# Performance work log

Hardware: AMD Instinct MI355X
Metric: run time of the kernel (lower is better)

## Reference

```python
import jax, jax.numpy as jnp
import numpy as np

N = 100000      # nodes
E = 3200000     # edges (avg degree 32)
DU = 256        # unary_channels
DP = 256        # pairwise_channels (== out_channels, required by fusion cat)
H = 64          # hidden_channels = out_channels // 4
DO = 256        # out_channels
STEPS = 1
EPS = 1e-5      # BatchNorm eps (torch default)


def _bn(h, gamma, beta):
    # BatchNorm1d, training-mode batch stats (biased variance, as torch normalizes)
    mu = jnp.mean(h, axis=0)
    var = jnp.var(h, axis=0)
    return gamma * (h - mu) * jax.lax.rsqrt(var + EPS) + beta


def setup_inputs() -> dict:
    key = jax.random.key(0)
    ks = jax.random.split(key, 12)
    edge_index = jax.random.randint(ks[0], (2, E), 0, N, dtype=jnp.int64)
    return {
        "x": jax.random.normal(ks[1], (N, DU), dtype=jnp.float32),
        "y": jax.random.normal(ks[2], (N, DP), dtype=jnp.float32),
        "pos": jax.random.normal(ks[3], (N, 3), dtype=jnp.float32),
        "edge_index": edge_index,
        "Wu": jax.random.normal(ks[4], (DU, H), dtype=jnp.float32) / np.sqrt(DU),
        "gu": jnp.ones((H,), jnp.float32), "bu": jnp.zeros((H,), jnp.float32),
        "Wp": jax.random.normal(ks[5], (DP, H), dtype=jnp.float32) / np.sqrt(DP),
        "gp": jnp.ones((H,), jnp.float32), "bp": jnp.zeros((H,), jnp.float32),
        "c": jnp.eye(H, dtype=jnp.float32) + 0.1 * jax.random.normal(ks[6], (H, H), dtype=jnp.float32),
        "Wm": jax.random.normal(ks[7], (H, DO), dtype=jnp.float32) / np.sqrt(H),
        "gm": jnp.ones((DO,), jnp.float32), "bm": jnp.zeros((DO,), jnp.float32),
        "Wf": jax.random.normal(ks[8], (2 * DO, DO), dtype=jnp.float32) / np.sqrt(2 * DO),
        "gf": jnp.ones((DO,), jnp.float32), "bf": jnp.zeros((DO,), jnp.float32),
    }


def reference(x, y, pos, edge_index, Wu, gu, bu, Wp, gp, bp, c, Wm, gm, bm, Wf, gf, bf):
    i, j = edge_index[0], edge_index[1]
    # unary / pairwise embeddings (Linear no-bias + BN)
    xu = _bn(x @ Wu, gu, bu)                      # [N, H]
    su = _bn(y @ Wp, gp, bp)                      # [N, H]
    # edge logits: -||s_i - s_j||^2, softmax grouped by destination i
    d = su[i] - su[j]                             # [E, H]
    logit = -jnp.sum(d * d, axis=1, keepdims=True)  # [E, 1]
    m = jax.ops.segment_max(logit, i, num_segments=N)
    ex = jnp.exp(logit - m[i])
    denom = jax.ops.segment_sum(ex, i, num_segments=N)
    s = ex / (denom[i] + 1e-16)                   # [E, 1] edge softmax weights
    # CRF mean-field iterations with linear solve
    z = xu
    C = c.T @ c                                   # [H, H]
    Minv = jnp.linalg.inv(jnp.eye(H, dtype=x.dtype) + C)
    h = xu
    for _ in range(STEPS):
        agg = jax.ops.segment_sum(s * h[j], i, num_segments=N)  # gather-scale-scatter
        h = (z + agg @ C) @ Minv
    # output heads
    h = jax.nn.leaky_relu(_bn(h @ Wm, gm, bm))
    out = jax.nn.leaky_relu(_bn(jnp.concatenate([h, y], axis=-1) @ Wf, gf, bf))
    return out
```

## Files before the change

kernel.cpp:

```cpp
#include <hip/hip_runtime.h>
#include <hip/hip_fp16.h>
#include <math.h>

typedef unsigned short u16;
typedef short s16x8 __attribute__((ext_vector_type(8)));
typedef unsigned short u16x8 __attribute__((ext_vector_type(8)));
typedef float f32x4 __attribute__((ext_vector_type(4)));

__device__ __forceinline__ float bf2f(u16 u) {
  unsigned x = ((unsigned)u) << 16;
  return __uint_as_float(x);
}
__device__ __forceinline__ u16 f2bf(float f) {
  unsigned x = __float_as_uint(f);
  unsigned r = x + 0x7FFFu + ((x >> 16) & 1u);
  return (u16)(r >> 16);
}

static const size_t OFF_MINV   = 0;
static const size_t OFF_AU     = 32ull * 1024;
static const size_t OFF_BUE    = 32ull * 1024 + 256;
static const size_t OFF_AP     = 32ull * 1024 + 512;
static const size_t OFF_APBE   = 32ull * 1024 + 768;
static const size_t OFF_AM     = 36ull * 1024;
static const size_t OFF_BM     = 37ull * 1024;
static const size_t OFF_AF     = 38ull * 1024;
static const size_t OFF_BF     = 39ull * 1024;
static const size_t OFF_BTOT   = 40ull * 1024;
static const size_t OFF_BOFF   = 44ull * 1024;
static const size_t OFF_WUT    = 64ull * 1024;
static const size_t OFF_WMT    = 128ull * 1024;
static const size_t OFF_WFT    = 192ull * 1024;
static const size_t OFF_WPH    = 512ull * 1024;
static const size_t OFF_WPL    = 576ull * 1024;
static const size_t OFF_PART1  = 1ull  * 1024 * 1024;
static const size_t OFF_PART2  = 2ull  * 1024 * 1024;
static const size_t OFF_ROWPTR = 3ull  * 1024 * 1024;
static const size_t OFF_BLKCNT = 5ull  * 1024 * 1024;
static const size_t OFF_SRCJ   = 18ull * 1024 * 1024;
static const size_t OFF_U      = 44ull * 1024 * 1024;
static const size_t OFF_P      = 70ull * 1024 * 1024;
static const size_t OFF_PS     = 109ull * 1024 * 1024;
static const size_t OFF_H2     = 122ull * 1024 * 1024;

#define NBLK_BIN 1024

__global__ __launch_bounds__(256) void k_prep(const float* __restrict__ c,
                                              float* __restrict__ minv_out) {
  __shared__ float CC[4096];
  __shared__ float aug[64 * 129];
  __shared__ float fs[64];
  float* cl = aug;
  int t = threadIdx.x;
  for (int idx = t; idx < 4096; idx += 256) cl[idx] = c[idx];
  __syncthreads();
  for (int idx = t; idx < 4096; idx += 256) {
    int a = idx >> 6, b = idx & 63;
    float s = (a == b) ? 1.f : 0.f;
    for (int k = 0; k < 64; ++k) s += cl[k * 64 + a] * cl[k * 64 + b];
    CC[idx] = s;
  }
  __syncthreads();
  for (int idx = t; idx < 8192; idx += 256) {
    int r = idx >> 7, cc = idx & 127;
    aug[r * 129 + cc] = (cc < 64) ? CC[r * 64 + cc] : (((cc - 64) == r) ? 1.f : 0.f);
  }
  __syncthreads();
  int cloc = t & 127;
  int rbase = t >> 7;
  for (int p = 0; p < 64; ++p) {
    float inv = 1.0f / aug[p * 129 + p];
    if (t < 64) fs[t] = (t == p) ? 0.f : aug[t * 129 + p];
    __syncthreads();
    if (t < 128) aug[p * 129 + t] *= inv;
    __syncthreads();
    float pc = aug[p * 129 + cloc];
#pragma unroll
    for (int rr = 0; rr < 64; rr += 2) {
      int r = rr + rbase;
      aug[r * 129 + cloc] -= fs[r] * pc;
    }
    __syncthreads();
  }
  for (int idx = t; idx < 4096; idx += 256) {
    int r = idx >> 6, cc = idx & 63;
    minv_out[idx] = aug[r * 129 + 64 + cc];
  }
}

__global__ __launch_bounds__(256) void k_tcvt_all(const float* __restrict__ Wu, const float* __restrict__ Wm,
                                                  const float* __restrict__ Wf, const float* __restrict__ Wp,
                                                  u16* __restrict__ WUT, u16* __restrict__ WMT,
                                                  u16* __restrict__ WFT, u16* __restrict__ WPH,
                                                  u16* __restrict__ WPL) {
  int b = blockIdx.x, t = threadIdx.x;
  if (b < 64) {
    int i = b * 256 + t;
    int k = i >> 6, n = i & 63;
    WUT[(size_t)n * 256 + k] = f2bf(Wu[i]);
  } else if (b < 128) {
    int i = (b - 64) * 256 + t;
    int k = i >> 8, n = i & 255;
    WMT[(size_t)n * 64 + k] = f2bf(Wm[i]);
  } else if (b < 640) {
    int i = (b - 128) * 256 + t;
    int k = i >> 8, n = i & 255;
    WFT[(size_t)n * 512 + k] = f2bf(Wf[i]);
  } else {
    int i = (b - 640) * 256 + t;
    int k = i >> 6, n = i & 63;
    float v = Wp[i];
    u16 h = f2bf(v);
    WPH[(size_t)n * 256 + k] = h;
    WPL[(size_t)n * 256 + k] = f2bf(v - bf2f(h));
  }
}

__global__ __launch_bounds__(256) void kA1(const int* __restrict__ ei, int E, int chunk,
                                           int* __restrict__ blockCnt, int nbk) {
  __shared__ int c[512];
  int t = threadIdx.x, bid = blockIdx.x;
  c[t] = 0; c[t + 256] = 0;
  __syncthreads();
  int e0 = bid * chunk, e1 = min(E, e0 + chunk);
  for (int e = e0 + t; e < e1; e += 256) atomicAdd(&c[ei[e] >> 8], 1);
  __syncthreads();
  for (int b = t; b < nbk; b += 256) blockCnt[(size_t)bid * nbk + b] = c[b];
}

__global__ __launch_bounds__(256) void kA2(int* __restrict__ blockCnt, int nbk,
                                           int* __restrict__ bucketTot) {
  int b = blockIdx.x, t = threadIdx.x;
  int base = t * 4;
  int v0 = blockCnt[(size_t)(base + 0) * nbk + b];
  int v1 = blockCnt[(size_t)(base + 1) * nbk + b];
  int v2 = blockCnt[(size_t)(base + 2) * nbk + b];
  int v3 = blockCnt[(size_t)(base + 3) * nbk + b];
  int s1 = v0 + v1, s2 = s1 + v2, tot = s2 + v3;
  __shared__ int ps[256];
  ps[t] = tot;
  __syncthreads();
  for (int off = 1; off < 256; off <<= 1) {
    int a = (t >= off) ? ps[t - off] : 0;
    __syncthreads();
    ps[t] += a;
    __syncthreads();
  }
  int ex = (t > 0) ? ps[t - 1] : 0;
  blockCnt[(size_t)(base + 0) * nbk + b] = ex;
  blockCnt[(size_t)(base + 1) * nbk + b] = ex + v0;
  blockCnt[(size_t)(base + 2) * nbk + b] = ex + s1;
  blockCnt[(size_t)(base + 3) * nbk + b] = ex + s2;
  if (t == 255) bucketTot[b] = ps[255];
}

__global__ __launch_bounds__(512) void kA2b(const int* __restrict__ bucketTot,
                                            int* __restrict__ bucketOff, int nbk) {
  __shared__ int s[512];
  int t = threadIdx.x;
  s[t] = (t < nbk) ? bucketTot[t] : 0;
  __syncthreads();
  for (int off = 1; off < 512; off <<= 1) {
    int a = (t >= off) ? s[t - off] : 0;
    __syncthreads();
    s[t] += a;
    __syncthreads();
  }
  if (t == 0) bucketOff[0] = 0;
  if (t < nbk) bucketOff[t + 1] = s[t];
}

__global__ __launch_bounds__(256) void kA3(const int* __restrict__ ei, const int* __restrict__ ej,
                                           int E, int chunk,
                                           const int* __restrict__ blockExc,
                                           const int* __restrict__ bucketOff,
                                           int nbk, unsigned* __restrict__ tmp) {
  __shared__ int c[512], off[512], gb[512], cur[512];
  __shared__ uint2 stage[4096];
  int t = threadIdx.x, bid = blockIdx.x;
  c[t] = 0; c[t + 256] = 0;
  __syncthreads();
  int e0 = bid * chunk, e1 = min(E, e0 + chunk);
  int m = e1 - e0;
  for (int e = e0 + t; e < e1; e += 256) atomicAdd(&c[ei[e] >> 8], 1);
  __syncthreads();
  int v0 = c[t], v1 = c[t + 256];
  off[t] = v0; off[t + 256] = v1;
  __syncthreads();
  for (int o = 1; o < 512; o <<= 1) {
    int a0 = (t >= o) ? off[t - o] : 0;
    int a1 = ((t + 256) >= o) ? off[t + 256 - o] : 0;
    __syncthreads();
    off[t] += a0; off[t + 256] += a1;
    __syncthreads();
  }
  int ex0 = off[t] - v0, ex1 = off[t + 256] - v1;
  if (t < nbk)
    gb[t] = bucketOff[t] + blockExc[(size_t)bid * nbk + t] - ex0;
  if (t + 256 < nbk)
    gb[t + 256] = bucketOff[t + 256] + blockExc[(size_t)bid * nbk + t + 256] - ex1;
  cur[t] = ex0; cur[t + 256] = ex1;
  __syncthreads();
  for (int e = e0 + t; e < e1; e += 256) {
    int i = ei[e];
    int p = atomicAdd(&cur[i >> 8], 1);
    stage[p] = make_uint2((unsigned)i, (unsigned)ej[e]);
  }
  __syncthreads();
  for (int s = t; s < m; s += 256) {
    uint2 v = stage[s];
    tmp[gb[v.x >> 8] + s] = ((v.x & 255u) << 24) | v.y;
  }
}

#define BCAP 12288
__global__ __launch_bounds__(256) void kB(const unsigned* __restrict__ tmp,
                                          const int* __restrict__ bucketOff,
                                          int nbk, int N, int E,
                                          int* __restrict__ rowptr, int* __restrict__ srcj) {
  __shared__ int cnt[256], sc[256], cur[256];
  __shared__ int jbuf[BCAP];
  int b = blockIdx.x, t = threadIdx.x;
  int nb0 = b << 8;
  int e0 = bucketOff[b], e1 = bucketOff[b + 1];
  int m = e1 - e0;
  cnt[t] = 0;
  __syncthreads();
  for (int s = t; s < m; s += 256) atomicAdd(&cnt[tmp[e0 + s] >> 24], 1);
  __syncthreads();
  int v = cnt[t];
  sc[t] = v;
  __syncthreads();
  for (int off = 1; off < 256; off <<= 1) {
    int a = (t >= off) ? sc[t - off] : 0;
    __syncthreads();
    sc[t] += a;
    __syncthreads();
  }
  int exc = sc[t] - v;
  cur[t] = exc;
  if (nb0 + t < N) rowptr[nb0 + t] = e0 + exc;
  if (b == nbk - 1 && t == 0) rowptr[N] = E;
  __syncthreads();
  for (int s = t; s < m; s += 256) {
    unsigned e = tmp[e0 + s];
    int p = atomicAdd(&cur[e >> 24], 1);
    if (p < BCAP) jbuf[p] = (int)(e & 0xFFFFFFu);
  }
  __syncthreads();
  for (int s = t; s < m; s += 256) srcj[e0 + s] = jbuf[s];
}

template<int BN, int AMODE, int OBF, int STATS>
__global__ __launch_bounds__(256) void k_mfma(const u16* __restrict__ Abf, const float* __restrict__ Af32,
                                              int ldA, int K, int M,
                                              const u16* __restrict__ h2, const float* __restrict__ yy,
                                              const float* __restrict__ am, const float* __restrict__ bm,
                                              const u16* __restrict__ Bt,
                                              float* __restrict__ Cf, u16* __restrict__ Cb, int ldC,
                                              int ncTot, float* __restrict__ p1, float* __restrict__ p2) {
  constexpr int WN  = BN / 2;
  constexpr int FN  = WN / 16;
  constexpr int NPB = BN / 32;
  __shared__ u16 lds[2][(128 + BN) * 64];

  int t = threadIdx.x;
  int wid = t >> 6, lane = t & 63;
  int wr = wid >> 1, wc = wid & 1;
  int lr = lane & 15, lk = lane >> 4;
  int m0 = blockIdx.x * 128;
  int n0 = blockIdx.y * BN;
  int nK = K >> 6;

  int sidx = t;
  u16x8 ra[4];
  u16x8 rb[NPB];

  f32x4 acc[4][FN];
#pragma unroll
  for (int m = 0; m < 4; ++m)
#pragma unroll
    for (int n = 0; n < FN; ++n) acc[m][n] = (f32x4){0.f, 0.f, 0.f, 0.f};

  auto loadTile = [&](int kk) {
    int kk0 = kk * 64;
#pragma unroll
    for (int p = 0; p < 4; ++p) {
      int idx = p * 256 + sidx;
      int r = idx >> 3, c8 = idx & 7;
      int row = m0 + r; if (row >= M) row = M - 1;
      int k = kk0 + c8 * 8;
      if constexpr (AMODE == 0) {
        ra[p] = *(const u16x8*)(Abf + (size_t)row * ldA + k);
      } else if constexpr (AMODE == 2) {
        const float* src = Af32 + (size_t)row * ldA + k;
        float4 a = *(const float4*)src;
        float4 b = *(const float4*)(src + 4);
        u16x8 o;
        o[0] = f2bf(a.x); o[1] = f2bf(a.y); o[2] = f2bf(a.z); o[3] = f2bf(a.w);
        o[4] = f2bf(b.x); o[5] = f2bf(b.y); o[6] = f2bf(b.z); o[7] = f2bf(b.w);
        ra[p] = o;
      } else {
        if (kk0 < 256) {
          u16x8 h8 = *(const u16x8*)(h2 + (size_t)row * 256 + k);
          float av[8], bv[8];
          *(float4*)(av)     = *(const float4*)(am + k);
          *(float4*)(av + 4) = *(const float4*)(am + k + 4);
          *(float4*)(bv)     = *(const float4*)(bm + k);
          *(float4*)(bv + 4) = *(const float4*)(bm + k + 4);
          u16x8 o;
#pragma unroll
          for (int j = 0; j < 8; ++j) {
            float v = bf2f((u16)h8[j]) * av[j] + bv[j];
            v = v > 0.f ? v : 0.01f * v;
            o[j] = f2bf(v);
          }
          ra[p] = o;
        } else {
          float yv[8];
          *(float4*)(yv)     = *(const float4*)(yy + (size_t)row * 256 + (k - 256));
          *(float4*)(yv + 4) = *(const float4*)(yy + (size_t)row * 256 + (k - 256) + 4);
          u16x8 o;
#pragma unroll
          for (int j = 0; j < 8; ++j) o[j] = f2bf(yv[j]);
          ra[p] = o;
        }
      }
    }
#pragma unroll
    for (int p = 0; p < NPB; ++p) {
      int idx = p * 256 + sidx;
      int r = idx >> 3, c8 = idx & 7;
      rb[p] = *(const u16x8*)(Bt + (size_t)(n0 + r) * K + kk0 + c8 * 8);
    }
  };

  auto dswrite = [&](int b) {
    char* As  = (char*)&lds[b][0];
    char* Bsc = As + 128 * 64 * 2;
#pragma unroll
    for (int p = 0; p < 4; ++p) {
      int idx = p * 256 + sidx;
      int r = idx >> 3, c8 = idx & 7;
      *(u16x8*)(As + r * 128 + ((c8 * 16) ^ ((r & 7) << 4))) = ra[p];
    }
#pragma unroll
    for (int p = 0; p < NPB; ++p) {
      int idx = p * 256 + sidx;
      int r = idx >> 3, c8 = idx & 7;
      *(u16x8*)(Bsc + r * 128 + ((c8 * 16) ^ ((r & 7) << 4))) = rb[p];
    }
  };

  auto compute = [&](int b) {
    const char* As  = (const char*)&lds[b][0];
    const char* Bsc = As + 128 * 64 * 2;
#pragma unroll
    for (int ks = 0; ks < 2; ++ks) {
      int kb = ks * 64 + lk * 16;
      s16x8 af[4], bfr[FN];
#pragma unroll
      for (int m = 0; m < 4; ++m) {
        int row = wr * 64 + m * 16 + lr;
        af[m] = *(const s16x8*)(As + row * 128 + (kb ^ ((row & 7) << 4)));
      }
#pragma unroll
      for (int n = 0; n < FN; ++n) {
        int row = wc * WN + n * 16 + lr;
        bfr[n] = *(const s16x8*)(Bsc + row * 128 + (kb ^ ((row & 7) << 4)));
      }
#pragma unroll
      for (int m = 0; m < 4; ++m)
#pragma unroll
        for (int n = 0; n < FN; ++n)
          acc[m][n] = __builtin_amdgcn_mfma_f32_16x16x32_bf16(af[m], bfr[n], acc[m][n], 0, 0, 0);
    }
  };

  loadTile(0);
  dswrite(0);
  __syncthreads();
  for (int kk = 0; kk < nK; ++kk) {
    int b = kk & 1;
    if (kk + 1 < nK) loadTile(kk + 1);
    compute(b);
    if (kk + 1 < nK) { dswrite(b ^ 1); __syncthreads(); }
  }

#pragma unroll
  for (int m = 0; m < 4; ++m) {
#pragma unroll
    for (int n = 0; n < FN; ++n) {
      int col = n0 + wc * WN + n * 16 + lr;
#pragma unroll
      for (int q = 0; q < 4; ++q) {
        int row = m0 + wr * 64 + m * 16 + lk * 4 + q;
        if (row < M) {
          if constexpr (OBF) Cb[(size_t)row * ldC + col] = f2bf(acc[m][n][q]);
          else               Cf[(size_t)row * ldC + col] = acc[m][n][q];
        }
      }
    }
  }

  if constexpr (STATS) {
    __syncthreads();
    float* sb = (float*)&lds[0][0];
#pragma unroll
    for (int n = 0; n < FN; ++n) {
      float s1 = 0.f, s2 = 0.f;
#pragma unroll
      for (int m = 0; m < 4; ++m)
#pragma unroll
        for (int q = 0; q < 4; ++q) {
          int row = m0 + wr * 64 + m * 16 + lk * 4 + q;
          float v = (row < M) ? acc[m][n][q] : 0.f;
          s1 += v; s2 += v * v;
        }
      s1 += __shfl_xor(s1, 16); s2 += __shfl_xor(s2, 16);
      s1 += __shfl_xor(s1, 32); s2 += __shfl_xor(s2, 32);
      if (lk == 0) {
        int c = wc * WN + n * 16 + lr;
        sb[(wr * BN + c) * 2 + 0] = s1;
        sb[(wr * BN + c) * 2 + 1] = s2;
      }
    }
    __syncthreads();
    if (t < BN) {
      float s1 = sb[t * 2]     + sb[(BN + t) * 2];
      float s2 = sb[t * 2 + 1] + sb[(BN + t) * 2 + 1];
      p1[(size_t)blockIdx.x * ncTot + n0 + t] = s1;
      p2[(size_t)blockIdx.x * ncTot + n0 + t] = s2;
    }
  }
}

__global__ __launch_bounds__(256) void k_mfma_split(const float* __restrict__ Af, int K, int M,
                                                    const u16* __restrict__ Bh, const u16* __restrict__ Bl,
                                                    float* __restrict__ Cf,
                                                    float* __restrict__ p1, float* __restrict__ p2) {
  __shared__ u16 sAh[128 * 64], sAl[128 * 64], sBh[64 * 64], sBl[64 * 64];
  int t = threadIdx.x;
  int wid = t >> 6, lane = t & 63;
  int wr = wid >> 1, wc = wid & 1;
  int lr = lane & 15, lk = lane >> 4;
  int m0 = blockIdx.x * 128;
  int nK = K >> 6;

  u16x8 rah[4], ral[4], rbh[2], rbl[2];
  f32x4 acc[4][2];
#pragma unroll
  for (int m = 0; m < 4; ++m)
#pragma unroll
    for (int n = 0; n < 2; ++n) acc[m][n] = (f32x4){0.f, 0.f, 0.f, 0.f};

  auto loadTile = [&](int kk) {
    int kk0 = kk * 64;
#pragma unroll
    for (int p = 0; p < 4; ++p) {
      int idx = p * 256 + t;
      int r = idx >> 3, c8 = idx & 7;
      int row = m0 + r; if (row >= M) row = M - 1;
      const float* src = Af + (size_t)row * K + kk0 + c8 * 8;
      float4 a = *(const float4*)src;
      float4 b = *(const float4*)(src + 4);
      float v[8];
      *(float4*)(v) = a; *(float4*)(v + 4) = b;
      u16x8 oh, ol;
#pragma unroll
      for (int j = 0; j < 8; ++j) {
        u16 h = f2bf(v[j]);
        oh[j] = h;
        ol[j] = f2bf(v[j] - bf2f(h));
      }
      rah[p] = oh; ral[p] = ol;
    }
#pragma unroll
    for (int p = 0; p < 2; ++p) {
      int idx = p * 256 + t;
      int r = idx >> 3, c8 = idx & 7;
      rbh[p] = *(const u16x8*)(Bh + (size_t)r * K + kk0 + c8 * 8);
      rbl[p] = *(const u16x8*)(Bl + (size_t)r * K + kk0 + c8 * 8);
    }
  };

  auto dswrite = [&]() {
    char* Ah = (char*)sAh; char* Al = (char*)sAl;
    char* Bhc = (char*)sBh; char* Blc = (char*)sBl;
#pragma unroll
    for (int p = 0; p < 4; ++p) {
      int idx = p * 256 + t;
      int r = idx >> 3, c8 = idx & 7;
      int off = r * 128 + ((c8 * 16) ^ ((r & 7) << 4));
      *(u16x8*)(Ah + off) = rah[p];
      *(u16x8*)(Al + off) = ral[p];
    }
#pragma unroll
    for (int p = 0; p < 2; ++p) {
      int idx = p * 256 + t;
      int r = idx >> 3, c8 = idx & 7;
      int off = r * 128 + ((c8 * 16) ^ ((r & 7) << 4));
      *(u16x8*)(Bhc + off) = rbh[p];
      *(u16x8*)(Blc + off) = rbl[p];
    }
  };

  auto compute = [&]() {
    const char* Ah = (const char*)sAh; const char* Al = (const char*)sAl;
    const char* Bhc = (const char*)sBh; const char* Blc = (const char*)sBl;
#pragma unroll
    for (int ks = 0; ks < 2; ++ks) {
      int kb = ks * 64 + lk * 16;
      s16x8 fah[4], fal[4], fbh[2], fbl[2];
#pragma unroll
      for (int m = 0; m < 4; ++m) {
        int row = wr * 64 + m * 16 + lr;
        int off = row * 128 + (kb ^ ((row & 7) << 4));
        fah[m] = *(const s16x8*)(Ah + off);
        fal[m] = *(const s16x8*)(Al + off);
      }
#pragma unroll
      for (int n = 0; n < 2; ++n) {
        int row = wc * 32 + n * 16 + lr;
        int off = row * 128 + (kb ^ ((row & 7) << 4));
        fbh[n] = *(const s16x8*)(Bhc + off);
        fbl[n] = *(const s16x8*)(Blc + off);
      }
#pragma unroll
      for (int m = 0; m < 4; ++m)
#pragma unroll
        for (int n = 0; n < 2; ++n) {
          acc[m][n] = __builtin_amdgcn_mfma_f32_16x16x32_bf16(fah[m], fbh[n], acc[m][n], 0, 0, 0);
          acc[m][n] = __builtin_amdgcn_mfma_f32_16x16x32_bf16(fah[m], fbl[n], acc[m][n], 0, 0, 0);
          acc[m][n] = __builtin_amdgcn_mfma_f32_16x16x32_bf16(fal[m], fbh[n], acc[m][n], 0, 0, 0);
        }
    }
  };

  loadTile(0);
  for (int kk = 0; kk < nK; ++kk) {
    __syncthreads();
    dswrite();
    __syncthreads();
    if (kk + 1 < nK) loadTile(kk + 1);
    compute();
  }

#pragma unroll
  for (int m = 0; m < 4; ++m) {
#pragma unroll
    for (int n = 0; n < 2; ++n) {
      int col = wc * 32 + n * 16 + lr;
#pragma unroll
      for (int q = 0; q < 4; ++q) {
        int row = m0 + wr * 64 + m * 16 + lk * 4 + q;
        if (row < M) Cf[(size_t)row * 64 + col] = acc[m][n][q];
      }
    }
  }

  __syncthreads();
  float* sb = (float*)sAh;
#pragma unroll
  for (int n = 0; n < 2; ++n) {
    float s1 = 0.f, s2 = 0.f;
#pragma unroll
    for (int m = 0; m < 4; ++m)
#pragma unroll
      for (int q = 0; q < 4; ++q) {
        int row = m0 + wr * 64 + m * 16 + lk * 4 + q;
        float v = (row < M) ? acc[m][n][q] : 0.f;
        s1 += v; s2 += v * v;
      }
    s1 += __shfl_xor(s1, 16); s2 += __shfl_xor(s2, 16);
    s1 += __shfl_xor(s1, 32); s2 += __shfl_xor(s2, 32);
    if (lk == 0) {
      int c = wc * 32 + n * 16 + lr;
      sb[(wr * 64 + c) * 2 + 0] = s1;
      sb[(wr * 64 + c) * 2 + 1] = s2;
    }
  }
  __syncthreads();
  if (t < 64) {
    float s1 = sb[t * 2]     + sb[(64 + t) * 2];
    float s2 = sb[t * 2 + 1] + sb[(64 + t) * 2 + 1];
    p1[(size_t)blockIdx.x * 64 + t] = s1;
    p2[(size_t)blockIdx.x * 64 + t] = s2;
  }
}

__global__ __launch_bounds__(256) void k_reduce_fin(const float* __restrict__ part1,
                                                    const float* __restrict__ part2,
                                                    int nb, int C, float invN,
                                                    const float* __restrict__ gamma,
                                                    const float* __restrict__ beta,
                                                    float* __restrict__ a_out,
                                                    float* __restrict__ b_out) {
  int c = blockIdx.x;
  int t = threadIdx.x;
  float s1 = 0.f, s2 = 0.f;
  for (int b = t; b < nb; b += 256) {
    s1 += part1[(size_t)b * C + c];
    s2 += part2[(size_t)b * C + c];
  }
  for (int m = 32; m; m >>= 1) { s1 += __shfl_xor(s1, m); s2 += __shfl_xor(s2, m); }
  __shared__ float l1[4], l2[4];
  if ((t & 63) == 0) { l1[t >> 6] = s1; l2[t >> 6] = s2; }
  __syncthreads();
  if (t == 0) {
    s1 = l1[0] + l1[1] + l1[2] + l1[3];
    s2 = l2[0] + l2[1] + l2[2] + l2[3];
    float mu  = s1 * invN;
    float var = s2 * invN - mu * mu;
    float a = gamma[c] * rsqrtf(var + 1e-5f);
    a_out[c] = a;
    b_out[c] = beta[c] - mu * a;
  }
}

__global__ __launch_bounds__(256) void k_scaleP(const float* __restrict__ P, const float* __restrict__ ap,
                                                __half* __restrict__ PS, int n8) {
  for (int i = blockIdx.x * 256 + threadIdx.x; i < n8; i += gridDim.x * 256) {
    int c0 = (i & 7) * 8;
    float4 s0 = *(const float4*)(ap + c0), s1 = *(const float4*)(ap + c0 + 4);
    float4 a = ((const float4*)P)[i * 2];
    float4 b = ((const float4*)P)[i * 2 + 1];
    __half2 o0 = __floats2half2_rn(a.x * s0.x, a.y * s0.y);
    __half2 o1 = __floats2half2_rn(a.z * s0.z, a.w * s0.w);
    __half2 o2 = __floats2half2_rn(b.x * s1.x, b.y * s1.y);
    __half2 o3 = __floats2half2_rn(b.z * s1.z, b.w * s1.w);
    uint4 out;
    out.x = *(unsigned*)&o0; out.y = *(unsigned*)&o1;
    out.z = *(unsigned*)&o2; out.w = *(unsigned*)&o3;
    ((uint4*)PS)[i] = out;
  }
}

__global__ __launch_bounds__(256) void k_nodeall(const __half* __restrict__ PS,
                                                 const int* __restrict__ srcj,
                                                 const int* __restrict__ rowptr,
                                                 const u16* __restrict__ UB,
                                                 const float* __restrict__ au,
                                                 const float* __restrict__ bue,
                                                 const float* __restrict__ minv,
                                                 int N, u16* __restrict__ HB) {
  __shared__ float mS[4096];
  __shared__ float zma[4][64];
  int t = threadIdx.x;
  for (int idx = t; idx < 1024; idx += 256)
    ((float4*)mS)[idx] = ((const float4*)minv)[idx];
  __syncthreads();

  int lane = t & 63, wid = t >> 6;
  int node = blockIdx.x * 4 + wid;
  if (node >= N) return;

  int lane8 = lane & 7, g8 = lane >> 3;
  const uint4* P4 = (const uint4*)PS;
  uint4 uv = P4[(size_t)node * 8 + lane8];
  float2 u0 = __half22float2(*(const __half2*)&uv.x);
  float2 u1 = __half22float2(((const __half2*)&uv.x)[1]);
  float2 u2 = __half22float2(*(const __half2*)&uv.z);
  float2 u3 = __half22float2(((const __half2*)&uv.z)[1]);
  float psl = __half2float(PS[(size_t)node * 64 + lane]);
  int b0 = rowptr[node], b1 = rowptr[node + 1];
  int deg = b1 - b0;
  float aggv = 0.f;
  if (deg > 0) {
    int cnt = deg < 64 ? deg : 64;
    int jj = (lane < cnt) ? srcj[b0 + lane] : 0;
    float lg = -INFINITY;
    int capbase = lane & ~7;
    int capsrc  = (lane & 7) << 3;
    for (int ss = 0; ss < cnt; ss += 8) {
      int sl = ss + g8; if (sl >= cnt) sl = cnt - 1;
      int j = __shfl(jj, sl);
      uint4 vv = P4[(size_t)j * 8 + lane8];
      float2 v0 = __half22float2(*(const __half2*)&vv.x);
      float2 v1 = __half22float2(((const __half2*)&vv.x)[1]);
      float2 v2 = __half22float2(*(const __half2*)&vv.z);
      float2 v3 = __half22float2(((const __half2*)&vv.z)[1]);
      float d0 = u0.x - v0.x, d1 = u0.y - v0.y;
      float d2 = u1.x - v1.x, d3 = u1.y - v1.y;
      float d4 = u2.x - v2.x, d5 = u2.y - v2.y;
      float d6 = u3.x - v3.x, d7 = u3.y - v3.y;
      float p = d0*d0 + d1*d1 + d2*d2 + d3*d3 + d4*d4 + d5*d5 + d6*d6 + d7*d7;
      p += __shfl_xor(p, 1, 8);
      p += __shfl_xor(p, 2, 8);
      p += __shfl_xor(p, 4, 8);
      float val = __shfl(p, capsrc);
      if (ss == capbase && lane < cnt) lg = -val;
    }
    float mx = lg;
    for (int s = b0 + 64; s < b1; ++s) {
      int j = srcj[s];
      float d = psl - __half2float(PS[(size_t)j * 64 + lane]);
      float p = d * d;
      for (int m = 32; m; m >>= 1) p += __shfl_xor(p, m);
      mx = fmaxf(mx, -p);
    }
    for (int m = 32; m; m >>= 1) mx = fmaxf(mx, __shfl_xor(mx, m));
    float ex = (lane < cnt) ? __expf(lg - mx) : 0.f;
    float sm = ex;
    for (int s = b0 + 64; s < b1; ++s) {
      int j = srcj[s];
      float d = psl - __half2float(PS[(size_t)j * 64 + lane]);
      float p = d * d;
      for (int m = 32; m; m >>= 1) p += __shfl_xor(p, m);
      if (lane == 0) sm += __expf(-p - mx);
    }
    for (int m = 32; m; m >>= 1) sm += __shfl_xor(sm, m);
    float inv = 1.0f / (sm + 1e-16f);
    float w = ex * inv;
    float acc = 0.f;
    int ss = 0;
    for (; ss + 8 <= cnt; ss += 8) {
      int   j0 = __shfl(jj, ss),     j1 = __shfl(jj, ss + 1);
      int   j2 = __shfl(jj, ss + 2), j3 = __shfl(jj, ss + 3);
      int   j4 = __shfl(jj, ss + 4), j5 = __shfl(jj, ss + 5);
      int   j6 = __shfl(jj, ss + 6), j7 = __shfl(jj, ss + 7);
      float w0 = __shfl(w, ss),      w1 = __shfl(w, ss + 1);
      float w2 = __shfl(w, ss + 2),  w3 = __shfl(w, ss + 3);
      float w4 = __shfl(w, ss + 4),  w5 = __shfl(w, ss + 5);
      float w6 = __shfl(w, ss + 6),  w7 = __shfl(w, ss + 7);
      float v0 = bf2f(UB[(size_t)j0 * 64 + lane]);
      float v1 = bf2f(UB[(size_t)j1 * 64 + lane]);
      float v2 = bf2f(UB[(size_t)j2 * 64 + lane]);
      float v3 = bf2f(UB[(size_t)j3 * 64 + lane]);
      float v4 = bf2f(UB[(size_t)j4 * 64 + lane]);
      float v5 = bf2f(UB[(size_t)j5 * 64 + lane]);
      float v6 = bf2f(UB[(size_t)j6 * 64 + lane]);
      float v7 = bf2f(UB[(size_t)j7 * 64 + lane]);
      acc += w0 * v0 + w1 * v1 + w2 * v2 + w3 * v3;
      acc += w4 * v4 + w5 * v5 + w6 * v6 + w7 * v7;
    }
    for (; ss < cnt; ++ss) {
      int j0 = __shfl(jj, ss);
      float w0 = __shfl(w, ss);
      acc += w0 * bf2f(UB[(size_t)j0 * 64 + lane]);
    }
    for (int s = b0 + 64; s < b1; ++s) {
      int j = srcj[s];
      float d = psl - __half2float(PS[(size_t)j * 64 + lane]);
      float p = d * d;
      for (int m = 32; m; m >>= 1) p += __shfl_xor(p, m);
      acc += __expf(-p - mx) * inv * bf2f(UB[(size_t)j * 64 + lane]);
    }
    aggv = au[lane] * acc + bue[lane];
  }
  float z = au[lane] * bf2f(UB[(size_t)node * 64 + lane]) + bue[lane];
  zma[wid][lane] = z - aggv;
  float h = aggv;
#pragma unroll 8
  for (int k = 0; k < 64; ++k) h += zma[wid][k] * mS[k * 64 + lane];
  HB[(size_t)node * 64 + lane] = f2bf(h);
}

__global__ __launch_bounds__(256) void k_bnact16(const u16* __restrict__ raw, const float* __restrict__ af,
                                                 const float* __restrict__ bfp, float* __restrict__ out, int n8) {
  int i = blockIdx.x * 256 + threadIdx.x;
  int stride = gridDim.x * 256;
  for (; i < n8; i += stride) {
    int c0 = (i & 31) * 8;
    float av[8], bv[8];
    *(float4*)(av) = *(const float4*)(af + c0);  *(float4*)(av + 4) = *(const float4*)(af + c0 + 4);
    *(float4*)(bv) = *(const float4*)(bfp + c0); *(float4*)(bv + 4) = *(const float4*)(bfp + c0 + 4);
    u16x8 r = ((const u16x8*)raw)[i];
    float o[8];
#pragma unroll
    for (int j = 0; j < 8; ++j) {
      float v = bf2f((u16)r[j]) * av[j] + bv[j];
      o[j] = (v > 0.f) ? v : 0.01f * v;
    }
    ((float4*)out)[i * 2]     = *(float4*)(o);
    ((float4*)out)[i * 2 + 1] = *(float4*)(o + 4);
  }
}

extern "C" void kernel_launch(void* const* d_in, const int* in_sizes, int n_in,
                              void* d_out, int out_size, void* d_ws, size_t ws_size,
                              hipStream_t stream) {
  const float* x    = (const float*)d_in[0];
  const float* y    = (const float*)d_in[1];
  const int*   eidx = (const int*)d_in[3];
  const float* Wu   = (const float*)d_in[4];
  const float* gu   = (const float*)d_in[5];
  const float* bu   = (const float*)d_in[6];
  const float* Wp   = (const float*)d_in[7];
  const float* gp   = (const float*)d_in[8];
  const float* bp   = (const float*)d_in[9];
  const float* cIn  = (const float*)d_in[10];
  const float* Wm   = (const float*)d_in[11];
  const float* gm   = (const float*)d_in[12];
  const float* bm   = (const float*)d_in[13];
  const float* Wf   = (const float*)d_in[14];
  const float* gf   = (const float*)d_in[15];
  const float* bfv  = (const float*)d_in[16];

  const int N = in_sizes[0] / 256;
  const int E = in_sizes[3] / 2;
  const int* ei = eidx;
  const int* ej = eidx + E;

  char* ws = (char*)d_ws;
  float* MINV  = (float*)(ws + OFF_MINV);
  float* AU    = (float*)(ws + OFF_AU);
  float* BUE   = (float*)(ws + OFF_BUE);
  float* AP    = (float*)(ws + OFF_AP);
  float* APBE  = (float*)(ws + OFF_APBE);
  float* AM    = (float*)(ws + OFF_AM);
  float* BM    = (float*)(ws + OFF_BM);
  float* AF    = (float*)(ws + OFF_AF);
  float* BF    = (float*)(ws + OFF_BF);
  int*   BTOT  = (int*)(ws + OFF_BTOT);
  int*   BOFF  = (int*)(ws + OFF_BOFF);
  u16*   WUT   = (u16*)(ws + OFF_WUT);
  u16*   WMT   = (u16*)(ws + OFF_WMT);
  u16*   WFT   = (u16*)(ws + OFF_WFT);
  u16*   WPH   = (u16*)(ws + OFF_WPH);
  u16*   WPL   = (u16*)(ws + OFF_WPL);
  float* PART1 = (float*)(ws + OFF_PART1);
  float* PART2 = (float*)(ws + OFF_PART2);
  int*   ROWPTR= (int*)(ws + OFF_ROWPTR);
  int*   BLKCNT= (int*)(ws + OFF_BLKCNT);
  u16*   HB    = (u16*)(ws + OFF_BLKCNT);
  int*   SRCJ  = (int*)(ws + OFF_SRCJ);
  u16*   RAWO  = (u16*)(ws + OFF_SRCJ);
  u16*   UBRAW = (u16*)(ws + OFF_U);
  unsigned* TMP= (unsigned*)(ws + OFF_P);
  float* P     = (float*)(ws + OFF_P);
  __half* PS   = (__half*)(ws + OFF_PS);
  u16*   H2    = (u16*)(ws + OFF_H2);

  const float invN = 1.0f / (float)N;
  const int mtiles   = (N + 127) / 128;
  const int n8_64    = N * 64 / 8;
  const int n8_256   = N * 256 / 8;
  const int nbk      = (N + 255) >> 8;
  const int chunk    = (E + NBLK_BIN - 1) / NBLK_BIN;

  k_prep<<<1, 256, 0, stream>>>(cIn, MINV);
  k_tcvt_all<<<704, 256, 0, stream>>>(Wu, Wm, Wf, Wp, WUT, WMT, WFT, WPH, WPL);

  kA1<<<NBLK_BIN, 256, 0, stream>>>(ei, E, chunk, BLKCNT, nbk);
  kA2<<<nbk, 256, 0, stream>>>(BLKCNT, nbk, BTOT);
  kA2b<<<1, 512, 0, stream>>>(BTOT, BOFF, nbk);
  kA3<<<NBLK_BIN, 256, 0, stream>>>(ei, ej, E, chunk, BLKCNT, BOFF, nbk, TMP);
  kB<<<nbk, 256, 0, stream>>>(TMP, BOFF, nbk, N, E, ROWPTR, SRCJ);

  k_mfma<64, 2, 1, 1><<<dim3(mtiles, 1), 256, 0, stream>>>(
      nullptr, x, 256, 256, N, nullptr, nullptr, nullptr, nullptr, WUT,
      nullptr, UBRAW, 64, 64, PART1, PART2);
  k_reduce_fin<<<64, 256, 0, stream>>>(PART1, PART2, mtiles, 64, invN, gu, bu, AU, BUE);

  k_mfma_split<<<mtiles, 256, 0, stream>>>(y, 256, N, WPH, WPL, P, PART1, PART2);
  k_reduce_fin<<<64, 256, 0, stream>>>(PART1, PART2, mtiles, 64, invN, gp, bp, AP, APBE);
  k_scaleP<<<1024, 256, 0, stream>>>(P, AP, PS, n8_64);

  k_nodeall<<<(N + 3) / 4, 256, 0, stream>>>(PS, SRCJ, ROWPTR, UBRAW, AU, BUE, MINV, N, HB);

  k_mfma<128, 0, 1, 1><<<dim3(mtiles, 2), 256, 0, stream>>>(
      HB, nullptr, 64, 64, N, nullptr, nullptr, nullptr, nullptr, WMT,
      nullptr, H2, 256, 256, PART1, PART2);
  k_reduce_fin<<<256, 256, 0, stream>>>(PART1, PART2, mtiles, 256, invN, gm, bm, AM, BM);

  k_mfma<128, 1, 1, 1><<<dim3(mtiles, 2), 256, 0, stream>>>(
      nullptr, nullptr, 0, 512, N, H2, y, AM, BM, WFT,
      nullptr, RAWO, 256, 256, PART1, PART2);
  k_reduce_fin<<<256, 256, 0, stream>>>(PART1, PART2, mtiles, 256, invN, gf, bfv, AF, BF);
  k_bnact16<<<2048, 256, 0, stream>>>(RAWO, AF, BF, (float*)d_out, n8_256);
}
```

Baseline: 550.5 us.

## Use full-width 512-thread GEMM tiles for output heads; simplify Gauss-Jordan pivoting

Adds a k_mfma2 kernel that computes a 128x256 output tile per block with 8 waves. This replaces the two-block-column grid for the Wm and Wf GEMMs, so the A operand (including the fused BN+leaky-relu transform of H2 and the y conversion) is loaded and converted once per row tile instead of twice. The small Minv inversion kernel also drops one barrier per pivot by deferring row normalisation to the final write. In exchange the new kernel uses more LDS per block (96 KB double-buffered) and more threads, which may reduce occupancy.

```diff
diff --git a/kernel.cpp b/kernel.cpp
--- a/kernel.cpp
+++ b/kernel.cpp
@@ -69,10 +69,7 @@
   int cloc = t & 127;
   int rbase = t >> 7;
   for (int p = 0; p < 64; ++p) {
-    float inv = 1.0f / aug[p * 129 + p];
-    if (t < 64) fs[t] = (t == p) ? 0.f : aug[t * 129 + p];
-    __syncthreads();
-    if (t < 128) aug[p * 129 + t] *= inv;
+    if (t < 64) fs[t] = (t == p) ? 0.f : aug[t * 129 + p] / aug[p * 129 + p];
     __syncthreads();
     float pc = aug[p * 129 + cloc];
 #pragma unroll
@@ -84,7 +81,7 @@
   }
   for (int idx = t; idx < 4096; idx += 256) {
     int r = idx >> 6, cc = idx & 63;
-    minv_out[idx] = aug[r * 129 + 64 + cc];
+    minv_out[idx] = aug[r * 129 + 64 + cc] / aug[r * 129 + r];
   }
 }
 
@@ -254,8 +251,6 @@
 template<int BN, int AMODE, int OBF, int STATS>
 __global__ __launch_bounds__(256) void k_mfma(const u16* __restrict__ Abf, const float* __restrict__ Af32,
                                               int ldA, int K, int M,
-                                              const u16* __restrict__ h2, const float* __restrict__ yy,
-                                              const float* __restrict__ am, const float* __restrict__ bm,
                                               const u16* __restrict__ Bt,
                                               float* __restrict__ Cf, u16* __restrict__ Cb, int ldC,
                                               int ncTot, float* __restrict__ p1, float* __restrict__ p2) {
@@ -292,7 +287,7 @@
       int k = kk0 + c8 * 8;
       if constexpr (AMODE == 0) {
         ra[p] = *(const u16x8*)(Abf + (size_t)row * ldA + k);
-      } else if constexpr (AMODE == 2) {
+      } else {
         const float* src = Af32 + (size_t)row * ldA + k;
         float4 a = *(const float4*)src;
         float4 b = *(const float4*)(src + 4);
@@ -300,6 +295,149 @@
         o[0] = f2bf(a.x); o[1] = f2bf(a.y); o[2] = f2bf(a.z); o[3] = f2bf(a.w);
         o[4] = f2bf(b.x); o[5] = f2bf(b.y); o[6] = f2bf(b.z); o[7] = f2bf(b.w);
         ra[p] = o;
+      }
+    }
+#pragma unroll
+    for (int p = 0; p < NPB; ++p) {
+      int idx = p * 256 + sidx;
+      int r = idx >> 3, c8 = idx & 7;
+      rb[p] = *(const u16x8*)(Bt + (size_t)(n0 + r) * K + kk0 + c8 * 8);
+    }
+  };
+
+  auto dswrite = [&](int b) {
+    char* As  = (char*)&lds[b][0];
+    char* Bsc = As + 128 * 64 * 2;
+#pragma unroll
+    for (int p = 0; p < 4; ++p) {
+      int idx = p * 256 + sidx;
+      int r = idx >> 3, c8 = idx & 7;
+      *(u16x8*)(As + r * 128 + ((c8 * 16) ^ ((r & 7) << 4))) = ra[p];
+    }
+#pragma unroll
+    for (int p = 0; p < NPB; ++p) {
+      int idx = p * 256 + sidx;
+      int r = idx >> 3, c8 = idx & 7;
+      *(u16x8*)(Bsc + r * 128 + ((c8 * 16) ^ ((r & 7) << 4))) = rb[p];
+    }
+  };
+
+  auto compute = [&](int b) {
+    const char* As  = (const char*)&lds[b][0];
+    const char* Bsc = As + 128 * 64 * 2;
+#pragma unroll
+    for (int ks = 0; ks < 2; ++ks) {
+      int kb = ks * 64 + lk * 16;
+      s16x8 af[4], bfr[FN];
+#pragma unroll
+      for (int m = 0; m < 4; ++m) {
+        int row = wr * 64 + m * 16 + lr;
+        af[m] = *(const s16x8*)(As + row * 128 + (kb ^ ((row & 7) << 4)));
+      }
+#pragma unroll
+      for (int n = 0; n < FN; ++n) {
+        int row = wc * WN + n * 16 + lr;
+        bfr[n] = *(const s16x8*)(Bsc + row * 128 + (kb ^ ((row & 7) << 4)));
+      }
+#pragma unroll
+      for (int m = 0; m < 4; ++m)
+#pragma unroll
+        for (int n = 0; n < FN; ++n)
+          acc[m][n] = __builtin_amdgcn_mfma_f32_16x16x32_bf16(af[m], bfr[n], acc[m][n], 0, 0, 0);
+    }
+  };
+
+  loadTile(0);
+  dswrite(0);
+  __syncthreads();
+  for (int kk = 0; kk < nK; ++kk) {
+    int b = kk & 1;
+    if (kk + 1 < nK) loadTile(kk + 1);
+    compute(b);
+    if (kk + 1 < nK) { dswrite(b ^ 1); __syncthreads(); }
+  }
+
+#pragma unroll
+  for (int m = 0; m < 4; ++m) {
+#pragma unroll
+    for (int n = 0; n < FN; ++n) {
+      int col = n0 + wc * WN + n * 16 + lr;
+#pragma unroll
+      for (int q = 0; q < 4; ++q) {
+        int row = m0 + wr * 64 + m * 16 + lk * 4 + q;
+        if (row < M) {
+          if constexpr (OBF) Cb[(size_t)row * ldC + col] = f2bf(acc[m][n][q]);
+          else               Cf[(size_t)row * ldC + col] = acc[m][n][q];
+        }
+      }
+    }
+  }
+
+  if constexpr (STATS) {
+    __syncthreads();
+    float* sb = (float*)&lds[0][0];
+#pragma unroll
+    for (int n = 0; n < FN; ++n) {
+      float s1 = 0.f, s2 = 0.f;
+#pragma unroll
+      for (int m = 0; m < 4; ++m)
+#pragma unroll
+        for (int q = 0; q < 4; ++q) {
+          int row = m0 + wr * 64 + m * 16 + lk * 4 + q;
+          float v = (row < M) ? acc[m][n][q] : 0.f;
+          s1 += v; s2 += v * v;
+        }
+      s1 += __shfl_xor(s1, 16); s2 += __shfl_xor(s2, 16);
+      s1 += __shfl_xor(s1, 32); s2 += __shfl_xor(s2, 32);
+      if (lk == 0) {
+        int c = wc * WN + n * 16 + lr;
+        sb[(wr * BN + c) * 2 + 0] = s1;
+        sb[(wr * BN + c) * 2 + 1] = s2;
+      }
+    }
+    __syncthreads();
+    if (t < BN) {
+      float s1 = sb[t * 2]     + sb[(BN + t) * 2];
+      float s2 = sb[t * 2 + 1] + sb[(BN + t) * 2 + 1];
+      p1[(size_t)blockIdx.x * ncTot + n0 + t] = s1;
+      p2[(size_t)blockIdx.x * ncTot + n0 + t] = s2;
+    }
+  }
+}
+
+template<int AMODE>
+__global__ __launch_bounds__(512) void k_mfma2(const u16* __restrict__ Abf, int ldA, int K, int M,
+                                               const u16* __restrict__ h2, const float* __restrict__ yy,
+                                               const float* __restrict__ am, const float* __restrict__ bm,
+                                               const u16* __restrict__ Bt,
+                                               u16* __restrict__ Cb,
+                                               float* __restrict__ p1, float* __restrict__ p2) {
+  __shared__ u16 lds[2][(128 + 256) * 64];
+  int t = threadIdx.x;
+  int wid = t >> 6, lane = t & 63;
+  int wr = wid >> 2, wc = wid & 3;
+  int lr = lane & 15, lk = lane >> 4;
+  int m0 = blockIdx.x * 128;
+  int nK = K >> 6;
+
+  u16x8 ra[2];
+  u16x8 rb[4];
+  f32x4 acc[4][4];
+#pragma unroll
+  for (int m = 0; m < 4; ++m)
+#pragma unroll
+    for (int n = 0; n < 4; ++n) acc[m][n] = (f32x4){0.f, 0.f, 0.f, 0.f};
+
+  auto loadTile = [&](int kk) {
+    int kk0 = kk * 64;
+#pragma unroll
+    for (int p = 0; p < 2; ++p) {
+      int idx = p * 512 + t;
+      int r = idx >> 3, c8 = idx & 7;
+      int row = m0 + r; if (row >= M) row = M - 1;
+      int k = kk0 + c8 * 8;
+      if constexpr (AMODE == 0) {
+        ra[p] = *(const u16x8*)(Abf + (size_t)row * ldA + k);
       } else {
         if (kk0 < 256) {
           u16x8 h8 = *(const u16x8*)(h2 + (size_t)row * 256 + k);
@@ -328,10 +466,10 @@
       }
     }
 #pragma unroll
-    for (int p = 0; p < NPB; ++p) {
-      int idx = p * 256 + sidx;
-      int r = idx >> 3, c8 = idx & 7;
-      rb[p] = *(const u16x8*)(Bt + (size_t)(n0 + r) * K + kk0 + c8 * 8);
+    for (int p = 0; p < 4; ++p) {
+      int idx = p * 512 + t;
+      int r = idx >> 3, c8 = idx & 7;
+      rb[p] = *(const u16x8*)(Bt + (size_t)r * K + kk0 + c8 * 8);
     }
   };
 
@@ -339,14 +477,14 @@
     char* As  = (char*)&lds[b][0];
     char* Bsc = As + 128 * 64 * 2;
 #pragma unroll
+    for (int p = 0; p < 2; ++p) {
+      int idx = p * 512 + t;
+      int r = idx >> 3, c8 = idx & 7;
+      *(u16x8*)(As + r * 128 + ((c8 * 16) ^ ((r & 7) << 4))) = ra[p];
+    }
+#pragma unroll
     for (int p = 0; p < 4; ++p) {
-      int idx = p * 256 + sidx;
-      int r = idx >> 3, c8 = idx & 7;
-      *(u16x8*)(As + r * 128 + ((c8 * 16) ^ ((r & 7) << 4))) = ra[p];
-    }
-#pragma unroll
-    for (int p = 0; p < NPB; ++p) {
-      int idx = p * 256 + sidx;
+      int idx = p * 512 + t;
       int r = idx >> 3, c8 = idx & 7;
       *(u16x8*)(Bsc + r * 128 + ((c8 * 16) ^ ((r & 7) << 4))) = rb[p];
     }
@@ -358,21 +496,21 @@
 #pragma unroll
     for (int ks = 0; ks < 2; ++ks) {
       int kb = ks * 64 + lk * 16;
-      s16x8 af[4], bfr[FN];
+      s16x8 af[4], bfr[4];
 #pragma unroll
       for (int m = 0; m < 4; ++m) {
         int row = wr * 64 + m * 16 + lr;
         af[m] = *(const s16x8*)(As + row * 128 + (kb ^ ((row & 7) << 4)));
       }
 #pragma unroll
-      for (int n = 0; n < FN; ++n) {
-        int row = wc * WN + n * 16 + lr;
+      for (int n = 0; n < 4; ++n) {
+        int row = wc * 64 + n * 16 + lr;
         bfr[n] = *(const s16x8*)(Bsc + row * 128 + (kb ^ ((row & 7) << 4)));
       }
 #pragma unroll
       for (int m = 0; m < 4; ++m)
 #pragma unroll
-        for (int n = 0; n < FN; ++n)
+        for (int n = 0; n < 4; ++n)
           acc[m][n] = __builtin_amdgcn_mfma_f32_16x16x32_bf16(af[m], bfr[n], acc[m][n], 0, 0, 0);
     }
   };
@@ -390,48 +528,43 @@
 #pragma unroll
   for (int m = 0; m < 4; ++m) {
 #pragma unroll
-    for (int n = 0; n < FN; ++n) {
-      int col = n0 + wc * WN + n * 16 + lr;
+    for (int n = 0; n < 4; ++n) {
+      int col = wc * 64 + n * 16 + lr;
 #pragma unroll
       for (int q = 0; q < 4; ++q) {
         int row = m0 + wr * 64 + m * 16 + lk * 4 + q;
-        if (row < M) {
-          if constexpr (OBF) Cb[(size_t)row * ldC + col] = f2bf(acc[m][n][q]);
-          else               Cf[(size_t)row * ldC + col] = acc[m][n][q];
-        }
-      }
-    }
-  }
-
-  if constexpr (STATS) {
-    __syncthreads();
-    float* sb = (float*)&lds[0][0];
-#pragma unroll
-    for (int n = 0; n < FN; ++n) {
-      float s1 = 0.f, s2 = 0.f;
-#pragma unroll
-      for (int m = 0; m < 4; ++m)
-#pragma unroll
-        for (int q = 0; q < 4; ++q) {
-          int row = m0 + wr * 64 + m * 16 + lk * 4 + q;
-          float v = (row < M) ? acc[m][n][q] : 0.f;
-          s1 += v; s2 += v * v;
-        }
-      s1 += __shfl_xor(s1, 16); s2 += __shfl_xor(s2, 16);
-      s1 += __shfl_xor(s1, 32); s2 += __shfl_xor(s2, 32);
-      if (lk == 0) {
-        int c = wc * WN + n * 16 + lr;
-        sb[(wr * BN + c) * 2 + 0] = s1;
-        sb[(wr * BN + c) * 2 + 1] = s2;
-      }
-    }
-    __syncthreads();
-    if (t < BN) {
-      float s1 = sb[t * 2]     + sb[(BN + t) * 2];
-      float s2 = sb[t * 2 + 1] + sb[(BN + t) * 2 + 1];
-      p1[(size_t)blockIdx.x * ncTot + n0 + t] = s1;
-      p2[(size_t)blockIdx.x * ncTot + n0 + t] = s2;
-    }
+        if (row < M) Cb[(size_t)row * 256 + col] = f2bf(acc[m][n][q]);
+      }
+    }
+  }
+
+  __syncthreads();
+  float* sb = (float*)&lds[0][0];
+#pragma unroll
+  for (int n = 0; n < 4; ++n) {
+    float s1 = 0.f, s2 = 0.f;
+#pragma unroll
+    for (int m = 0; m < 4; ++m)
+#pragma unroll
+      for (int q = 0; q < 4; ++q) {
+        int row = m0 + wr * 64 + m * 16 + lk * 4 + q;
+        float v = (row < M) ? acc[m][n][q] : 0.f;
+        s1 += v; s2 += v * v;
+      }
+    s1 += __shfl_xor(s1, 16); s2 += __shfl_xor(s2, 16);
+    s1 += __shfl_xor(s1, 32); s2 += __shfl_xor(s2, 32);
+    if (lk == 0) {
+      int c = wc * 64 + n * 16 + lr;
+      sb[(wr * 256 + c) * 2 + 0] = s1;
+      sb[(wr * 256 + c) * 2 + 1] = s2;
+    }
+  }
+  __syncthreads();
+  if (t < 256) {
+    float s1 = sb[t * 2]     + sb[(256 + t) * 2];
+    float s2 = sb[t * 2 + 1] + sb[(256 + t) * 2 + 1];
+    p1[(size_t)blockIdx.x * 256 + t] = s1;
+    p2[(size_t)blockIdx.x * 256 + t] = s2;
   }
 }
 
@@ -849,8 +982,7 @@
   kB<<<nbk, 256, 0, stream>>>(TMP, BOFF, nbk, N, E, ROWPTR, SRCJ);
 
   k_mfma<64, 2, 1, 1><<<dim3(mtiles, 1), 256, 0, stream>>>(
-      nullptr, x, 256, 256, N, nullptr, nullptr, nullptr, nullptr, WUT,
-      nullptr, UBRAW, 64, 64, PART1, PART2);
+      nullptr, x, 256, 256, N, WUT, nullptr, UBRAW, 64, 64, PART1, PART2);
   k_reduce_fin<<<64, 256, 0, stream>>>(PART1, PART2, mtiles, 64, invN, gu, bu, AU, BUE);
 
   k_mfma_split<<<mtiles, 256, 0, stream>>>(y, 256, N, WPH, WPL, P, PART1, PART2);
@@ -859,14 +991,12 @@
 
   k_nodeall<<<(N + 3) / 4, 256, 0, stream>>>(PS, SRCJ, ROWPTR, UBRAW, AU, BUE, MINV, N, HB);
 
-  k_mfma<128, 0, 1, 1><<<dim3(mtiles, 2), 256, 0, stream>>>(
-      HB, nullptr, 64, 64, N, nullptr, nullptr, nullptr, nullptr, WMT,
-      nullptr, H2, 256, 256, PART1, PART2);
+  k_mfma2<0><<<mtiles, 512, 0, stream>>>(
+      HB, 64, 64, N, nullptr, nullptr, nullptr, nullptr, WMT, H2, PART1, PART2);
   k_reduce_fin<<<256, 256, 0, stream>>>(PART1, PART2, mtiles, 256, invN, gm, bm, AM, BM);
 
-  k_mfma<128, 1, 1, 1><<<dim3(mtiles, 2), 256, 0, stream>>>(
-      nullptr, nullptr, 0, 512, N, H2, y, AM, BM, WFT,
-      nullptr, RAWO, 256, 256, PART1, PART2);
+  k_mfma2<1><<<mtiles, 512, 0, stream>>>(
+      nullptr, 0, 512, N, H2, y, AM, BM, WFT, RAWO, PART1, PART2);
   k_reduce_fin<<<256, 256, 0, stream>>>(PART1, PART2, mtiles, 256, invN, gf, bfv, AF, BF);
   k_bnact16<<<2048, 256, 0, stream>>>(RAWO, AF, BF, (float*)d_out, n8_256);
 }
```

New measurement: 536.7 us. 2.5% less time.
